# Optimization experiments

Measured on AMD Instinct MI355X. Metric: run time of the kernel, lower is better.

## Reference

```python
import jax, jax.numpy as jnp
import numpy as np
from jax import lax

DIM = 128
TOPW = 4
SCALE = DIM ** (-0.5)


def setup_inputs() -> dict:
    key = jax.random.key(0)
    kq, ki = jax.random.split(key)
    query = jax.random.normal(kq, (4, 4096, DIM), dtype=jnp.float32)
    image = jax.random.normal(ki, (4, 8192, DIM), dtype=jnp.float32)
    return {"query": query, "image": image}


def reference(query, image):
    # diff_routing=False: inputs are detached in torch; no effect on fwd values.
    # attn: (b, Nq, mn) = scaled QK^T
    attn = jnp.einsum('bqc,bmc->bqm', query, image) * SCALE
    _, topw_index = lax.top_k(attn, TOPW)  # (b, Nq, topw)
    return topw_index
```

## Files before the change

kernel.cpp:

```cpp
#include <hip/hip_runtime.h>
#include <float.h>
#include <stdint.h>


#define NBATCH 4
#define NQ 4096
#define NM 8192
#define KD 128

typedef unsigned short ushort_t;
typedef __attribute__((ext_vector_type(8))) short bf16x8;
typedef __attribute__((ext_vector_type(4))) float f32x4;

#define BETTER64(v, i, w, j) (((v) > (w)) || ((v) == (w) && (i) < (j)))

__device__ inline float fmed3(float a, float b, float c) {
#if __has_builtin(__builtin_amdgcn_fmed3f)
  return __builtin_amdgcn_fmed3f(a, b, c);
#else
  return fmaxf(fminf(a, b), fminf(fmaxf(a, b), c));
#endif
}

__device__ inline ushort_t f2bf(float f) {
  unsigned u = __float_as_uint(f);
  u += 0x7fffu + ((u >> 16) & 1u);
  return (ushort_t)(u >> 16);
}

__global__ __launch_bounds__(256) void wr_cvt(const float* __restrict__ qry,
                                              const float* __restrict__ img,
                                              ushort_t* __restrict__ qb,
                                              int4* __restrict__ ib) {
  const int blk = (int)blockIdx.x;
  const int tid = (int)threadIdx.x;
  if (blk < 2048) {
    const int t = blk * 256 + tid;
    const float4 v = ((const float4*)qry)[t];
    ushort4 o;
    o.x = f2bf(v.x); o.y = f2bf(v.y); o.z = f2bf(v.z); o.w = f2bf(v.w);
    ((ushort4*)qb)[t] = o;
  } else {
    const int tg = blk - 2048;
    const int b = tg >> 8;
    const int tile = tg & 255;
    __shared__ __align__(16) ushort_t T[32 * 128];
    {
      const int r = tid >> 3;
      const int seg = tid & 7;
      const float* src = img + ((size_t)(b * NM + tile * 32 + r)) * KD + seg * 16;
      ushort_t tmp[16];
#pragma unroll
      for (int i = 0; i < 4; ++i) {
        const float4 v = ((const float4*)src)[i];
        tmp[i * 4 + 0] = f2bf(v.x);
        tmp[i * 4 + 1] = f2bf(v.y);
        tmp[i * 4 + 2] = f2bf(v.z);
        tmp[i * 4 + 3] = f2bf(v.w);
      }
      const int c0 = (seg * 16 + r * 8) & 127;
      const int c1 = (seg * 16 + 8 + r * 8) & 127;
      *(int4*)&T[r * 128 + c0] = *(const int4*)&tmp[0];
      *(int4*)&T[r * 128 + c1] = *(const int4*)&tmp[8];
    }
    __syncthreads();
    int4* dstt = ib + ((size_t)b * 256 + tile) * 512;
#pragma unroll
    for (int h = 0; h < 2; ++h) {
      const int n = tid + h * 256;
      const int l = n & 63;
      const int ks = (n >> 6) & 3;
      const int htl = n >> 8;
      const int row = htl * 16 + (l & 15);
      const int col = ks * 32 + (l >> 4) * 8;
      dstt[n] = *(const int4*)&T[row * 128 + ((col + row * 8) & 127)];
    }
  }
}

__global__ __launch_bounds__(512, 2) void wr_mfma(const float* __restrict__ qry,
                                                  const float* __restrict__ img,
                                                  const ushort_t* __restrict__ qb,
                                                  const int4* __restrict__ ib,
                                                  int* __restrict__ out) {
  const int bid = (int)blockIdx.x;
  const int b = (bid & 7) >> 1;
  const int qt = ((bid >> 3) << 1) | (bid & 1);
  const int qbase = qt * 32;

  const int tid = (int)threadIdx.x;
  const int lane = tid & 63;
  const int w = tid >> 6;
  const int q15 = lane & 15;
  const int quad = lane >> 4;

  const ushort_t* Qb = qb + ((size_t)b * NQ + qbase) * KD;
  const int4* ibc = ib + (size_t)b * 131072;

  bf16x8 bfrag0[4], bfrag1[4];
#pragma unroll
  for (int ks = 0; ks < 4; ++ks) {
    bfrag0[ks] = *(const bf16x8*)(Qb + (size_t)q15 * KD + ks * 32 + quad * 8);
    bfrag1[ks] = *(const bf16x8*)(Qb + (size_t)(16 + q15) * KD + ks * 32 + quad * 8);
  }

  float tq0[4], tq1[4];
#pragma unroll
  for (int s = 0; s < 4; ++s) { tq0[s] = -FLT_MAX; tq1[s] = -FLT_MAX; }

  bf16x8 B0[4], B1[4], B2[4];

  auto loadH = [&](bf16x8* R, int h) {
    const int4* p = ibc + (((w * 64 + h) << 8) + lane);
#pragma unroll
    for (int ks = 0; ks < 4; ++ks) R[ks] = *(const bf16x8*)(p + ks * 64);
  };

  int hl = 3;
  int vb = 2047 - 4 * quad;

  auto step = [&](bf16x8* R) {
    f32x4 a0 = {0.f, 0.f, 0.f, 0.f}, a1 = {0.f, 0.f, 0.f, 0.f};
#pragma unroll
    for (int ks = 0; ks < 4; ++ks) {
      a0 = __builtin_amdgcn_mfma_f32_16x16x32_bf16(R[ks], bfrag0[ks], a0, 0, 0, 0);
      a1 = __builtin_amdgcn_mfma_f32_16x16x32_bf16(R[ks], bfrag1[ks], a1, 0, 0, 0);
    }
    if (hl < 64) loadH(R, hl);
    ++hl;
#pragma unroll
    for (int r = 0; r < 4; ++r) {
      const unsigned kr = (unsigned)(vb - r);
      const float ka =
          __uint_as_float((__float_as_uint(a0[r]) & 0xFFFFF800u) | kr);
      tq0[3] = fmed3(ka, tq0[2], tq0[3]);
      tq0[2] = fmed3(ka, tq0[1], tq0[2]);
      tq0[1] = fmed3(ka, tq0[0], tq0[1]);
      tq0[0] = fmaxf(tq0[0], ka);
      const float kb =
          __uint_as_float((__float_as_uint(a1[r]) & 0xFFFFF800u) | kr);
      tq1[3] = fmed3(kb, tq1[2], tq1[3]);
      tq1[2] = fmed3(kb, tq1[1], tq1[2]);
      tq1[1] = fmed3(kb, tq1[0], tq1[1]);
      tq1[0] = fmaxf(tq1[0], kb);
    }
    vb -= 16;
  };

  loadH(B0, 0);
  loadH(B1, 1);
  loadH(B2, 2);
  for (int g = 0; g < 21; ++g) { step(B0); step(B1); step(B2); }
  step(B0);

  {
    float k4[4];
#pragma unroll
    for (int e = 0; e < 4; ++e) k4[e] = __shfl_down(tq0[e], 32, 64);
#pragma unroll
    for (int e = 0; e < 4; ++e) {
      const float k = k4[e];
      tq0[3] = fmed3(k, tq0[2], tq0[3]);
      tq0[2] = fmed3(k, tq0[1], tq0[2]);
      tq0[1] = fmed3(k, tq0[0], tq0[1]);
      tq0[0] = fmaxf(tq0[0], k);
    }
#pragma unroll
    for (int e = 0; e < 4; ++e) k4[e] = __shfl_down(tq0[e], 16, 64);
#pragma unroll
    for (int e = 0; e < 4; ++e) {
      const float k = k4[e];
      tq0[3] = fmed3(k, tq0[2], tq0[3]);
      tq0[2] = fmed3(k, tq0[1], tq0[2]);
      tq0[1] = fmed3(k, tq0[0], tq0[1]);
      tq0[0] = fmaxf(tq0[0], k);
    }
#pragma unroll
    for (int e = 0; e < 4; ++e) k4[e] = __shfl_down(tq1[e], 32, 64);
#pragma unroll
    for (int e = 0; e < 4; ++e) {
      const float k = k4[e];
      tq1[3] = fmed3(k, tq1[2], tq1[3]);
      tq1[2] = fmed3(k, tq1[1], tq1[2]);
      tq1[1] = fmed3(k, tq1[0], tq1[1]);
      tq1[0] = fmaxf(tq1[0], k);
    }
#pragma unroll
    for (int e = 0; e < 4; ++e) k4[e] = __shfl_down(tq1[e], 16, 64);
#pragma unroll
    for (int e = 0; e < 4; ++e) {
      const float k = k4[e];
      tq1[3] = fmed3(k, tq1[2], tq1[3]);
      tq1[2] = fmed3(k, tq1[1], tq1[2]);
      tq1[1] = fmed3(k, tq1[0], tq1[1]);
      tq1[0] = fmaxf(tq1[0], k);
    }
  }

  __shared__ float ck[32][33];
  __shared__ int top8[32][8];
  __shared__ double pd[32][8];
  __shared__ int pi[32][8];

  if (lane < 16) {
#pragma unroll
    for (int s = 0; s < 4; ++s) {
      ck[q15][w * 4 + s] = tq0[s];
      ck[16 + q15][w * 4 + s] = tq1[s];
    }
  }
  __syncthreads();

  for (int p = tid; p < 1024; p += 512) {
    const int q = p >> 5;
    const int j = p & 31;
    const float k = ck[q][j];
    int rank = 0;
#pragma unroll 8
    for (int i = 0; i < 32; ++i) {
      const float o = ck[q][i];
      rank += (o > k) || (o == k && i < j);
    }
    if (rank < 8) {
      const unsigned bits = __float_as_uint(k);
      top8[q][rank] = (j >> 2) * 1024 + 2047 - (int)(bits & 0x7FFu);
    }
  }
  __syncthreads();

  if (tid < 256) {
    const int q = tid >> 3;
    const int slot = tid & 7;
    const int m = top8[q][slot];
    const float* qrow = qry + ((size_t)b * NQ + qbase + q) * KD;
    const float* irow = img + ((size_t)b * NM + m) * KD;
    double s0 = 0.0, s1 = 0.0, s2 = 0.0, s3 = 0.0;
#pragma unroll
    for (int k = 0; k < KD; k += 4) {
      const float4 xv = *(const float4*)(qrow + k);
      const float4 yv = *(const float4*)(irow + k);
      s0 = fma((double)xv.x, (double)yv.x, s0);
      s1 = fma((double)xv.y, (double)yv.y, s1);
      s2 = fma((double)xv.z, (double)yv.z, s2);
      s3 = fma((double)xv.w, (double)yv.w, s3);
    }
    pd[q][slot] = (s0 + s1) + (s2 + s3);
    pi[q][slot] = m;
  }
  __syncthreads();

  if (tid < 32) {
    const int q = tid;
    double fv[4];
    int fi[4];
#pragma unroll
    for (int e = 0; e < 4; ++e) { fv[e] = -DBL_MAX; fi[e] = 0x7fffffff; }
    for (int sl = 0; sl < 8; ++sl) {
      const double v = pd[q][sl];
      const int m = pi[q][sl];
      const bool b0 = BETTER64(v, m, fv[0], fi[0]);
      const bool b1 = BETTER64(v, m, fv[1], fi[1]);
      const bool b2 = BETTER64(v, m, fv[2], fi[2]);
      const bool b3 = BETTER64(v, m, fv[3], fi[3]);
      fv[3] = b2 ? fv[2] : (b3 ? v : fv[3]);
      fi[3] = b2 ? fi[2] : (b3 ? m : fi[3]);
      fv[2] = b1 ? fv[1] : (b2 ? v : fv[2]);
      fi[2] = b1 ? fi[1] : (b2 ? m : fi[2]);
      fv[1] = b0 ? fv[0] : (b1 ? v : fv[1]);
      fi[1] = b0 ? fi[0] : (b1 ? m : fi[1]);
      fv[0] = b0 ? v : fv[0];
      fi[0] = b0 ? m : fi[0];
    }
    int4 o;
    o.x = fi[0]; o.y = fi[1]; o.z = fi[2]; o.w = fi[3];
    *(int4*)(out + ((size_t)b * NQ + qbase + q) * 4) = o;
  }
}

#define QT 64
#define MT 128
#define KC 64
#define NTHREADS 512

__global__ __launch_bounds__(NTHREADS) void wr_main(const float* __restrict__ qry,
                                                    const float* __restrict__ img,
                                                    int* __restrict__ out) {
  __shared__ __align__(16) float A_lds[KD * QT];
  __shared__ __align__(16) float B_lds[KC * MT];

  const int t = (int)threadIdx.x;
  const int b = (int)blockIdx.x >> 6;
  const int qbase = ((int)blockIdx.x & 63) * QT;

  const float* qp = qry + ((size_t)b * NQ + qbase) * KD;
  const float* ip = img + (size_t)b * NM * KD;

  {
    const int r = t >> 3;
    const int kc = t & 7;
    const float* src = qp + (size_t)r * KD;
#pragma unroll
    for (int i = 0; i < 4; ++i) {
      const int k0 = kc * 4 + i * 32;
      const float4 v = *(const float4*)(src + k0);
      A_lds[(k0 + 0) * QT + r] = v.x;
      A_lds[(k0 + 1) * QT + r] = v.y;
      A_lds[(k0 + 2) * QT + r] = v.z;
      A_lds[(k0 + 3) * QT + r] = v.w;
    }
  }

  const int qi = t >> 5;
  const int mi = t & 31;

  float tv[4][4];
  int ti[4][4];
#pragma unroll
  for (int j = 0; j < 4; ++j)
#pragma unroll
    for (int s = 0; s < 4; ++s) { tv[j][s] = -FLT_MAX; ti[j][s] = 0x7fffffff; }

  for (int tile = 0; tile < NM / MT; ++tile) {
    const int mbase = tile * MT;
    float acc[4][4];
#pragma unroll
    for (int j = 0; j < 4; ++j)
#pragma unroll
      for (int s = 0; s < 4; ++s) acc[j][s] = 0.0f;

    for (int kb = 0; kb < KD; kb += KC) {
      __syncthreads();
      {
        const int r = t >> 2;
        const int kc = t & 3;
        const float* src = ip + (size_t)(mbase + r) * KD + kb;
#pragma unroll
        for (int i = 0; i < 4; ++i) {
          const int k0 = kc * 4 + i * 16;
          const float4 v = *(const float4*)(src + k0);
          B_lds[(k0 + 0) * MT + r] = v.x;
          B_lds[(k0 + 1) * MT + r] = v.y;
          B_lds[(k0 + 2) * MT + r] = v.z;
          B_lds[(k0 + 3) * MT + r] = v.w;
        }
      }
      __syncthreads();

#pragma unroll 8
      for (int k = 0; k < KC; ++k) {
        const float4 av = *(const float4*)&A_lds[(kb + k) * QT + qi * 4];
        const float4 bv = *(const float4*)&B_lds[k * MT + mi * 4];
        acc[0][0] = fmaf(av.x, bv.x, acc[0][0]);
        acc[0][1] = fmaf(av.x, bv.y, acc[0][1]);
        acc[0][2] = fmaf(av.x, bv.z, acc[0][2]);
        acc[0][3] = fmaf(av.x, bv.w, acc[0][3]);
        acc[1][0] = fmaf(av.y, bv.x, acc[1][0]);
        acc[1][1] = fmaf(av.y, bv.y, acc[1][1]);
        acc[1][2] = fmaf(av.y, bv.z, acc[1][2]);
        acc[1][3] = fmaf(av.y, bv.w, acc[1][3]);
        acc[2][0] = fmaf(av.z, bv.x, acc[2][0]);
        acc[2][1] = fmaf(av.z, bv.y, acc[2][1]);
        acc[2][2] = fmaf(av.z, bv.z, acc[2][2]);
        acc[2][3] = fmaf(av.z, bv.w, acc[2][3]);
        acc[3][0] = fmaf(av.w, bv.x, acc[3][0]);
        acc[3][1] = fmaf(av.w, bv.y, acc[3][1]);
        acc[3][2] = fmaf(av.w, bv.z, acc[3][2]);
        acc[3][3] = fmaf(av.w, bv.w, acc[3][3]);
      }
    }

#pragma unroll
    for (int j = 0; j < 4; ++j) {
#pragma unroll
      for (int s = 0; s < 4; ++s) {
        const float v = acc[j][s];
        const int m = mbase + mi * 4 + s;
        const bool b0 = v > tv[j][0];
        const bool b1 = v > tv[j][1];
        const bool b2 = v > tv[j][2];
        const bool b3 = v > tv[j][3];
        tv[j][3] = b2 ? tv[j][2] : (b3 ? v : tv[j][3]);
        ti[j][3] = b2 ? ti[j][2] : (b3 ? m : ti[j][3]);
        tv[j][2] = b1 ? tv[j][1] : (b2 ? v : tv[j][2]);
        ti[j][2] = b1 ? ti[j][1] : (b2 ? m : ti[j][2]);
        tv[j][1] = b0 ? tv[j][0] : (b1 ? v : tv[j][1]);
        ti[j][1] = b0 ? ti[j][0] : (b1 ? m : ti[j][1]);
        tv[j][0] = b0 ? v : tv[j][0];
        ti[j][0] = b0 ? m : ti[j][0];
      }
    }
  }

  __syncthreads();
  int* idx_lds = (int*)B_lds;
#pragma unroll
  for (int j = 0; j < 4; ++j)
#pragma unroll
    for (int s = 0; s < 4; ++s)
      idx_lds[(qi * 4 + j) * 128 + mi * 4 + s] = ti[j][s];
  __syncthreads();

  double* pv = (double*)A_lds;
  int* piL = (int*)(A_lds + 4096);
  {
    const int r = t >> 3;
    const int slot = t & 7;
    const float* qrow = qp + (size_t)r * KD;
    double bv[4];
    int bi[4];
#pragma unroll
    for (int e = 0; e < 4; ++e) { bv[e] = -DBL_MAX; bi[e] = 0x7fffffff; }

    for (int c = 0; c < 16; ++c) {
      const int m = idx_lds[r * 128 + slot * 16 + c];
      const float* irow = ip + (size_t)m * KD;
      double s0 = 0.0, s1 = 0.0, s2 = 0.0, s3 = 0.0;
#pragma unroll
      for (int k = 0; k < KD; k += 4) {
        const float4 xv = *(const float4*)(qrow + k);
        const float4 yv = *(const float4*)(irow + k);
        s0 = fma((double)xv.x, (double)yv.x, s0);
        s1 = fma((double)xv.y, (double)yv.y, s1);
        s2 = fma((double)xv.z, (double)yv.z, s2);
        s3 = fma((double)xv.w, (double)yv.w, s3);
      }
      const double v = (s0 + s1) + (s2 + s3);
      const bool b0 = BETTER64(v, m, bv[0], bi[0]);
      const bool b1 = BETTER64(v, m, bv[1], bi[1]);
      const bool b2 = BETTER64(v, m, bv[2], bi[2]);
      const bool b3 = BETTER64(v, m, bv[3], bi[3]);
      bv[3] = b2 ? bv[2] : (b3 ? v : bv[3]);
      bi[3] = b2 ? bi[2] : (b3 ? m : bi[3]);
      bv[2] = b1 ? bv[1] : (b2 ? v : bv[2]);
      bi[2] = b1 ? bi[1] : (b2 ? m : bi[2]);
      bv[1] = b0 ? bv[0] : (b1 ? v : bv[1]);
      bi[1] = b0 ? bi[0] : (b1 ? m : bi[1]);
      bv[0] = b0 ? v : bv[0];
      bi[0] = b0 ? m : bi[0];
    }
#pragma unroll
    for (int e = 0; e < 4; ++e) {
      pv[t * 4 + e] = bv[e];
      piL[t * 4 + e] = bi[e];
    }
  }
  __syncthreads();

  if (t < QT) {
    double fv[4];
    int fi[4];
#pragma unroll
    for (int e = 0; e < 4; ++e) { fv[e] = -DBL_MAX; fi[e] = 0x7fffffff; }
    for (int sl = 0; sl < 8; ++sl) {
#pragma unroll
      for (int e = 0; e < 4; ++e) {
        const double v = pv[(t * 8 + sl) * 4 + e];
        const int m = piL[(t * 8 + sl) * 4 + e];
        const bool b0 = BETTER64(v, m, fv[0], fi[0]);
        const bool b1 = BETTER64(v, m, fv[1], fi[1]);
        const bool b2 = BETTER64(v, m, fv[2], fi[2]);
        const bool b3 = BETTER64(v, m, fv[3], fi[3]);
        fv[3] = b2 ? fv[2] : (b3 ? v : fv[3]);
        fi[3] = b2 ? fi[2] : (b3 ? m : fi[3]);
        fv[2] = b1 ? fv[1] : (b2 ? v : fv[2]);
        fi[2] = b1 ? fi[1] : (b2 ? m : fi[2]);
        fv[1] = b0 ? fv[0] : (b1 ? v : fv[1]);
        fi[1] = b0 ? fi[0] : (b1 ? m : fi[1]);
        fv[0] = b0 ? v : fv[0];
        fi[0] = b0 ? m : fi[0];
      }
    }
    int4 o;
    o.x = fi[0]; o.y = fi[1]; o.z = fi[2]; o.w = fi[3];
    *(int4*)(out + ((size_t)b * NQ + qbase + t) * 4) = o;
  }
}

extern "C" void kernel_launch(void* const* d_in, const int* in_sizes, int n_in,
                              void* d_out, int out_size, void* d_ws, size_t ws_size,
                              hipStream_t stream) {
  const float* qry = (const float*)d_in[0];
  const float* img = (const float*)d_in[1];
  int* out = (int*)d_out;

  const size_t qbBytes = (size_t)NBATCH * NQ * KD * sizeof(ushort_t);
  const size_t ibBytes = (size_t)NBATCH * NM * KD * sizeof(ushort_t);

  if (ws_size >= qbBytes + ibBytes) {
    ushort_t* qb = (ushort_t*)d_ws;
    int4* ib = (int4*)((char*)d_ws + qbBytes);
    wr_cvt<<<3072, 256, 0, stream>>>(qry, img, qb, ib);
    wr_mfma<<<512, 512, 0, stream>>>(qry, img, qb, ib, out);
  } else {
    wr_main<<<NBATCH * (NQ / QT), NTHREADS, 0, stream>>>(qry, img, out);
  }
}
```

Measured before the change: 138.9 us.

## Process 64 queries per block to reuse image fragments across four MFMA tiles

Each block now handles 64 query rows instead of 32, issuing four 16x16 MFMAs per loaded image fragment instead of two. This halves the image-matrix reads from global/L2 per query and halves the grid to 256 blocks, with launch bounds lowered to one block per CU. The cost is more registers for query fragments and top-k state, and fewer resident waves to hide latency; 256 blocks may also underfill a 256-CU device less evenly.

```diff
diff --git a/kernel.cpp b/kernel.cpp
--- a/kernel.cpp
+++ b/kernel.cpp
@@ -78,7 +78,7 @@
   }
 }
 
-__global__ __launch_bounds__(512, 2) void wr_mfma(const float* __restrict__ qry,
+__global__ __launch_bounds__(512, 1) void wr_mfma(const float* __restrict__ qry,
                                                   const float* __restrict__ img,
                                                   const ushort_t* __restrict__ qb,
                                                   const int4* __restrict__ ib,
@@ -86,7 +86,7 @@
   const int bid = (int)blockIdx.x;
   const int b = (bid & 7) >> 1;
   const int qt = ((bid >> 3) << 1) | (bid & 1);
-  const int qbase = qt * 32;
+  const int qbase = qt * 64;
 
   const int tid = (int)threadIdx.x;
   const int lane = tid & 63;
@@ -97,16 +97,19 @@
   const ushort_t* Qb = qb + ((size_t)b * NQ + qbase) * KD;
   const int4* ibc = ib + (size_t)b * 131072;
 
-  bf16x8 bfrag0[4], bfrag1[4];
-#pragma unroll
-  for (int ks = 0; ks < 4; ++ks) {
-    bfrag0[ks] = *(const bf16x8*)(Qb + (size_t)q15 * KD + ks * 32 + quad * 8);
-    bfrag1[ks] = *(const bf16x8*)(Qb + (size_t)(16 + q15) * KD + ks * 32 + quad * 8);
-  }
-
-  float tq0[4], tq1[4];
-#pragma unroll
-  for (int s = 0; s < 4; ++s) { tq0[s] = -FLT_MAX; tq1[s] = -FLT_MAX; }
+  bf16x8 bfrag[4][4];
+#pragma unroll
+  for (int s = 0; s < 4; ++s)
+#pragma unroll
+    for (int ks = 0; ks < 4; ++ks)
+      bfrag[s][ks] =
+          *(const bf16x8*)(Qb + (size_t)(s * 16 + q15) * KD + ks * 32 + quad * 8);
+
+  float tch[4][4];
+#pragma unroll
+  for (int s = 0; s < 4; ++s)
+#pragma unroll
+    for (int e = 0; e < 4; ++e) tch[s][e] = -FLT_MAX;
 
   bf16x8 B0[4], B1[4], B2[4];
 
@@ -120,29 +123,29 @@
   int vb = 2047 - 4 * quad;
 
   auto step = [&](bf16x8* R) {
-    f32x4 a0 = {0.f, 0.f, 0.f, 0.f}, a1 = {0.f, 0.f, 0.f, 0.f};
-#pragma unroll
-    for (int ks = 0; ks < 4; ++ks) {
-      a0 = __builtin_amdgcn_mfma_f32_16x16x32_bf16(R[ks], bfrag0[ks], a0, 0, 0, 0);
-      a1 = __builtin_amdgcn_mfma_f32_16x16x32_bf16(R[ks], bfrag1[ks], a1, 0, 0, 0);
-    }
+    f32x4 a[4];
+#pragma unroll
+    for (int s = 0; s < 4; ++s) a[s] = {0.f, 0.f, 0.f, 0.f};
+#pragma unroll
+    for (int ks = 0; ks < 4; ++ks)
+#pragma unroll
+      for (int s = 0; s < 4; ++s)
+        a[s] = __builtin_amdgcn_mfma_f32_16x16x32_bf16(R[ks], bfrag[s][ks], a[s],
+                                                       0, 0, 0);
     if (hl < 64) loadH(R, hl);
     ++hl;
 #pragma unroll
-    for (int r = 0; r < 4; ++r) {
-      const unsigned kr = (unsigned)(vb - r);
-      const float ka =
-          __uint_as_float((__float_as_uint(a0[r]) & 0xFFFFF800u) | kr);
-      tq0[3] = fmed3(ka, tq0[2], tq0[3]);
-      tq0[2] = fmed3(ka, tq0[1], tq0[2]);
-      tq0[1] = fmed3(ka, tq0[0], tq0[1]);
-      tq0[0] = fmaxf(tq0[0], ka);
-      const float kb =
-          __uint_as_float((__float_as_uint(a1[r]) & 0xFFFFF800u) | kr);
-      tq1[3] = fmed3(kb, tq1[2], tq1[3]);
-      tq1[2] = fmed3(kb, tq1[1], tq1[2]);
-      tq1[1] = fmed3(kb, tq1[0], tq1[1]);
-      tq1[0] = fmaxf(tq1[0], kb);
+    for (int s = 0; s < 4; ++s) {
+#pragma unroll
+      for (int r = 0; r < 4; ++r) {
+        const unsigned kr = (unsigned)(vb - r);
+        const float k =
+            __uint_as_float((__float_as_uint(a[s][r]) & 0xFFFFF800u) | kr);
+        tch[s][3] = fmed3(k, tch[s][2], tch[s][3]);
+        tch[s][2] = fmed3(k, tch[s][1], tch[s][2]);
+        tch[s][1] = fmed3(k, tch[s][0], tch[s][1]);
+        tch[s][0] = fmaxf(tch[s][0], k);
+      }
     }
     vb -= 16;
   };
@@ -153,65 +156,45 @@
   for (int g = 0; g < 21; ++g) { step(B0); step(B1); step(B2); }
   step(B0);
 
-  {
+#pragma unroll
+  for (int s = 0; s < 4; ++s) {
     float k4[4];
 #pragma unroll
-    for (int e = 0; e < 4; ++e) k4[e] = __shfl_down(tq0[e], 32, 64);
+    for (int e = 0; e < 4; ++e) k4[e] = __shfl_down(tch[s][e], 32, 64);
 #pragma unroll
     for (int e = 0; e < 4; ++e) {
       const float k = k4[e];
-      tq0[3] = fmed3(k, tq0[2], tq0[3]);
-      tq0[2] = fmed3(k, tq0[1], tq0[2]);
-      tq0[1] = fmed3(k, tq0[0], tq0[1]);
-      tq0[0] = fmaxf(tq0[0], k);
-    }
-#pragma unroll
-    for (int e = 0; e < 4; ++e) k4[e] = __shfl_down(tq0[e], 16, 64);
+      tch[s][3] = fmed3(k, tch[s][2], tch[s][3]);
+      tch[s][2] = fmed3(k, tch[s][1], tch[s][2]);
+      tch[s][1] = fmed3(k, tch[s][0], tch[s][1]);
+      tch[s][0] = fmaxf(tch[s][0], k);
+    }
+#pragma unroll
+    for (int e = 0; e < 4; ++e) k4[e] = __shfl_down(tch[s][e], 16, 64);
 #pragma unroll
     for (int e = 0; e < 4; ++e) {
       const float k = k4[e];
-      tq0[3] = fmed3(k, tq0[2], tq0[3]);
-      tq0[2] = fmed3(k, tq0[1], tq0[2]);
-      tq0[1] = fmed3(k, tq0[0], tq0[1]);
-      tq0[0] = fmaxf(tq0[0], k);
-    }
-#pragma unroll
-    for (int e = 0; e < 4; ++e) k4[e] = __shfl_down(tq1[e], 32, 64);
-#pragma unroll
-    for (int e = 0; e < 4; ++e) {
-      const float k = k4[e];
-      tq1[3] = fmed3(k, tq1[2], tq1[3]);
-      tq1[2] = fmed3(k, tq1[1], tq1[2]);
-      tq1[1] = fmed3(k, tq1[0], tq1[1]);
-      tq1[0] = fmaxf(tq1[0], k);
-    }
-#pragma unroll
-    for (int e = 0; e < 4; ++e) k4[e] = __shfl_down(tq1[e], 16, 64);
-#pragma unroll
-    for (int e = 0; e < 4; ++e) {
-      const float k = k4[e];
-      tq1[3] = fmed3(k, tq1[2], tq1[3]);
-      tq1[2] = fmed3(k, tq1[1], tq1[2]);
-      tq1[1] = fmed3(k, tq1[0], tq1[1]);
-      tq1[0] = fmaxf(tq1[0], k);
-    }
-  }
-
-  __shared__ float ck[32][33];
-  __shared__ int top8[32][8];
-  __shared__ double pd[32][8];
-  __shared__ int pi[32][8];
+      tch[s][3] = fmed3(k, tch[s][2], tch[s][3]);
+      tch[s][2] = fmed3(k, tch[s][1], tch[s][2]);
+      tch[s][1] = fmed3(k, tch[s][0], tch[s][1]);
+      tch[s][0] = fmaxf(tch[s][0], k);
+    }
+  }
+
+  __shared__ float ck[64][33];
+  __shared__ int top8[64][8];
+  __shared__ double pd[64][8];
+  __shared__ int pi[64][8];
 
   if (lane < 16) {
 #pragma unroll
-    for (int s = 0; s < 4; ++s) {
-      ck[q15][w * 4 + s] = tq0[s];
-      ck[16 + q15][w * 4 + s] = tq1[s];
-    }
-  }
-  __syncthreads();
-
-  for (int p = tid; p < 1024; p += 512) {
+    for (int s = 0; s < 4; ++s)
+#pragma unroll
+      for (int e = 0; e < 4; ++e) ck[s * 16 + q15][w * 4 + e] = tch[s][e];
+  }
+  __syncthreads();
+
+  for (int p = tid; p < 2048; p += 512) {
     const int q = p >> 5;
     const int j = p & 31;
     const float k = ck[q][j];
@@ -228,7 +211,7 @@
   }
   __syncthreads();
 
-  if (tid < 256) {
+  {
     const int q = tid >> 3;
     const int slot = tid & 7;
     const int m = top8[q][slot];
@@ -249,7 +232,7 @@
   }
   __syncthreads();
 
-  if (tid < 32) {
+  if (tid < 64) {
     const int q = tid;
     double fv[4];
     int fi[4];
@@ -490,7 +473,7 @@
     ushort_t* qb = (ushort_t*)d_ws;
     int4* ib = (int4*)((char*)d_ws + qbBytes);
     wr_cvt<<<3072, 256, 0, stream>>>(qry, img, qb, ib);
-    wr_mfma<<<512, 512, 0, stream>>>(qry, img, qb, ib, out);
+    wr_mfma<<<256, 512, 0, stream>>>(qry, img, qb, ib, out);
   } else {
     wr_main<<<NBATCH * (NQ / QT), NTHREADS, 0, stream>>>(qry, img, out);
   }
```

Measured after the change: 133.0 us. 4.2% less time.
